# Kernel tuning notes

Hardware: AMD Instinct MI355X
Metric: run time of the kernel (lower is better)

The kernel has to match this reference:

```python
import jax, jax.numpy as jnp
import numpy as np

S, B, T = 16, 32, 64        # max_sents, batch, max_tokens
V, E, H = 50000, 256, 256   # vocab, embed_size, gru_hidden (n_dim)
NC = 50                     # n_classes


def setup_inputs() -> dict:
    key = jax.random.key(0)
    ks = jax.random.split(key, 30)

    def u(k, shape, s=0.1):
        return jax.random.uniform(k, shape, minval=-s, maxval=s, dtype=jnp.float32)

    return {
        "x": jax.random.randint(ks[0], (S, B, T), 0, V, dtype=jnp.int64),
        "embed": jax.random.normal(ks[1], (V, E), dtype=jnp.float32) * 0.1,
        # word-level bi-GRU (input E, hidden H); gate order r,z,n as in torch
        "wg_Wih_f": u(ks[2], (3 * H, E)), "wg_Whh_f": u(ks[3], (3 * H, H)),
        "wg_bih_f": u(ks[4], (3 * H,)),   "wg_bhh_f": u(ks[5], (3 * H,)),
        "wg_Wih_b": u(ks[6], (3 * H, E)), "wg_Whh_b": u(ks[7], (3 * H, H)),
        "wg_bih_b": u(ks[8], (3 * H,)),   "wg_bhh_b": u(ks[9], (3 * H,)),
        "word_W": u(ks[10], (2 * H, 2 * H)),
        "word_b": u(ks[11], (2 * H, 1)),
        "word_proj": u(ks[12], (2 * H, 1)),
        # sentence-level bi-GRU (input 2H, hidden H)
        "sg_Wih_f": u(ks[13], (3 * H, 2 * H)), "sg_Whh_f": u(ks[14], (3 * H, H)),
        "sg_bih_f": u(ks[15], (3 * H,)),       "sg_bhh_f": u(ks[16], (3 * H,)),
        "sg_Wih_b": u(ks[17], (3 * H, 2 * H)), "sg_Whh_b": u(ks[18], (3 * H, H)),
        "sg_bih_b": u(ks[19], (3 * H,)),       "sg_bhh_b": u(ks[20], (3 * H,)),
        "sent_W": u(ks[21], (2 * H, 2 * H)),
        "sent_b": u(ks[22], (2 * H, 1)),
        "sent_proj": u(ks[23], (2 * H, 1)),
        "fin_W": u(ks[24], (NC, 2 * H)),
        "fin_b": u(ks[25], (NC,)),
        "state_word": jnp.zeros((2, B, H), dtype=jnp.float32),
        "state_sent": jnp.zeros((2, B, H), dtype=jnp.float32),
    }


def _gru_dir(x, h0, Wih, Whh, bih, bhh, reverse=False):
    # x: [T, B, in]; returns hidden states [T, B, H] (in original time order)
    xp = jnp.einsum('tbe,ge->tbg', x, Wih) + bih  # precompute input projections

    def step(h, xt):
        g = h @ Whh.T + bhh
        xr, xz, xn = jnp.split(xt, 3, axis=-1)
        hr, hz, hn = jnp.split(g, 3, axis=-1)
        r = jax.nn.sigmoid(xr + hr)
        z = jax.nn.sigmoid(xz + hz)
        n = jnp.tanh(xn + r * hn)
        h = (1.0 - z) * n + z * h
        return h, h

    _, hs = jax.lax.scan(step, h0, xp, reverse=reverse)
    return hs


def _bigru(x, h0, Wf, Hf, bif, bhf, Wb, Hb, bib, bhb):
    f = _gru_dir(x, h0[0], Wf, Hf, bif, bhf, reverse=False)
    b = _gru_dir(x, h0[1], Wb, Hb, bib, bhb, reverse=True)
    return jnp.concatenate([f, b], axis=-1)  # [T, B, 2H]


def _attn_pool(out, W, b, proj):
    # out: [T, B, 2H]; batch_matmul_bias(tanh) -> batch_matmul -> softmax over T -> weighted sum
    squish = jnp.tanh(jnp.einsum('tbh,hk->tbk', out, W) + b[:, 0])  # [T,B,2H]
    scores = jnp.einsum('tbk,k->tb', squish, proj[:, 0])            # [T,B]
    a = jax.nn.softmax(scores, axis=0)                              # softmax over seq
    return jnp.einsum('tb,tbh->bh', a, out)                         # [B,2H]


def reference(x, embed,
              wg_Wih_f, wg_Whh_f, wg_bih_f, wg_bhh_f,
              wg_Wih_b, wg_Whh_b, wg_bih_b, wg_bhh_b,
              word_W, word_b, word_proj,
              sg_Wih_f, sg_Whh_f, sg_bih_f, sg_bhh_f,
              sg_Wih_b, sg_Whh_b, sg_bih_b, sg_bhh_b,
              sent_W, sent_b, sent_proj,
              fin_W, fin_b, state_word, state_sent):
    e = embed[x]                         # [S,B,T,E]
    e = jnp.transpose(e, (0, 2, 1, 3))   # [S,T,B,E] (torch code transposes per sentence)

    word_out = jax.vmap(
        lambda xs: _bigru(xs, state_word,
                          wg_Wih_f, wg_Whh_f, wg_bih_f, wg_bhh_f,
                          wg_Wih_b, wg_Whh_b, wg_bih_b, wg_bhh_b)
    )(e)                                 # [S,T,B,2H]

    s = jax.vmap(lambda o: _attn_pool(o, word_W, word_b, word_proj))(word_out)  # [S,B,2H]

    sent_out = _bigru(s, state_sent,
                      sg_Wih_f, sg_Whh_f, sg_bih_f, sg_bhh_f,
                      sg_Wih_b, sg_Whh_b, sg_bih_b, sg_bhh_b)  # [S,B,2H]
    pooled = _attn_pool(sent_out, sent_W, sent_b, sent_proj)   # [B,2H]
    return pooled @ fin_W.T + fin_b                            # [B,NC] logits
```

## Files before the change

### kernel.cpp

```cpp
#include <hip/hip_runtime.h>


typedef float  f32x4  __attribute__((ext_vector_type(4)));
typedef int    i32x4  __attribute__((ext_vector_type(4)));
typedef __bf16 bf16x8 __attribute__((ext_vector_type(8)));

#define DEVINL static __device__ __forceinline__

DEVINL unsigned short f2bf(float f) {
    unsigned int x = __builtin_bit_cast(unsigned int, f);
    x = x + 0x7fffu + ((x >> 16) & 1u);
    return (unsigned short)(x >> 16);
}
DEVINL float bf2f(unsigned short u) {
    unsigned int x = ((unsigned int)u) << 16;
    return __builtin_bit_cast(float, x);
}
DEVINL float bfe16(unsigned int v, int hi) {
    return bf2f((unsigned short)(hi ? (v >> 16) : (v & 0xffffu)));
}
DEVINL float sigm(float x) { return __builtin_amdgcn_rcpf(1.f + __expf(-x)); }
DEVINL float tanh_(float x) {
    x = fminf(fmaxf(x, -20.f), 20.f);
    float e = __expf(-2.f * x);
    return (1.f - e) * __builtin_amdgcn_rcpf(1.f + e);
}
DEVINL void mfma16(f32x4& acc, i32x4 a, i32x4 b) {
    acc = __builtin_amdgcn_mfma_f32_16x16x32_bf16(
        __builtin_bit_cast(bf16x8, a), __builtin_bit_cast(bf16x8, b), acc, 0, 0, 0);
}
DEVINL f32x4 zero4() { f32x4 v = {0.f, 0.f, 0.f, 0.f}; return v; }

#define O_WPWF    ((size_t)0)
#define O_WPWB    ((size_t)1048576)
#define O_WPSGIH  ((size_t)2097152)
#define O_WPSHHF  ((size_t)3670016)
#define O_WPSHHB  ((size_t)4063232)
#define O_WPWW    ((size_t)4456448)
#define O_WPSW    ((size_t)4980736)
#define O_BIASWF  ((size_t)5505024)
#define O_BIASWB  ((size_t)5509120)
#define O_BIHCAT  ((size_t)5513216)
#define O_WOUT    ((size_t)5519360)
#define O_SCORESW ((size_t)39073792)
#define O_SSFRAG  ((size_t)39204864)
#define O_XPSENT  ((size_t)39729152)
#define O_SOFRAG  ((size_t)42874880)
#define O_SCORESS ((size_t)43399168)
#define WS_NEED_B ((size_t)43401216)
#define O_XPW     ((size_t)43401216)
#define WS_NEED_A ((size_t)144064512)

__global__ void k_prep(const float* wihf, const float* whhf,
                       const float* wihb, const float* whhb,
                       const float* sgihf, const float* sgihb,
                       const float* sghhf, const float* sghhb,
                       const float* wordW, const float* sentW,
                       const float* bihf, const float* bhhf,
                       const float* bihb, const float* bhhb,
                       const float* sgbihf, const float* sgbihb,
                       const float* sgbhhf, const float* sgbhhb,
                       unsigned short* Wpwf, unsigned short* Wpwb,
                       unsigned short* Wpsgih,
                       unsigned short* WpshhF, unsigned short* WpshhB,
                       unsigned short* WpwW, unsigned short* WpsW,
                       float* biasWf, float* biasWb, float* bihCat)
{
    const int tid0 = blockIdx.x * blockDim.x + threadIdx.x;
    const int nth  = gridDim.x * blockDim.x;

    for (int idx = tid0; idx < 2 * 524288; idx += nth) {
        int d = idx >> 19, sidx = idx & 524287;
        int j = sidx & 7, chunk = sidx >> 3;
        int lane = chunk & 63, nk = chunk >> 6;
        int kf = nk & 15, nf = nk >> 4;
        int n = nf * 16 + (lane & 15);
        int k = kf * 32 + (lane >> 4) * 8 + j;
        const float* Wih = d ? wihb : wihf;
        const float* Whh = d ? whhb : whhf;
        int g4 = n >> 8, jj = n & 255;
        float v = 0.f;
        if (k < 256) {
            if (g4 == 0) v = Wih[jj * 256 + k];
            else if (g4 == 1) v = Wih[(256 + jj) * 256 + k];
            else if (g4 == 2) v = Wih[(512 + jj) * 256 + k];
        } else {
            int kk = k - 256;
            if (g4 == 0) v = Whh[jj * 256 + kk];
            else if (g4 == 1) v = Whh[(256 + jj) * 256 + kk];
            else if (g4 == 3) v = Whh[(512 + jj) * 256 + kk];
        }
        (d ? Wpwb : Wpwf)[sidx] = f2bf(v);
    }
    for (int idx = tid0; idx < 786432; idx += nth) {
        int j = idx & 7, chunk = idx >> 3;
        int lane = chunk & 63, nk = chunk >> 6;
        int kf = nk & 15, nf = nk >> 4;
        int n = nf * 16 + (lane & 15);
        int k = kf * 32 + (lane >> 4) * 8 + j;
        float v = (n < 768) ? sgihf[n * 512 + k] : sgihb[(n - 768) * 512 + k];
        Wpsgih[idx] = f2bf(v);
    }
    for (int idx = tid0; idx < 2 * 196608; idx += nth) {
        int d = idx >= 196608;
        int sidx = d ? idx - 196608 : idx;
        int j = sidx & 7, chunk = sidx >> 3;
        int lane = chunk & 63, nk = chunk >> 6;
        int kf = nk & 7, nf = nk >> 3;
        int n = nf * 16 + (lane & 15);
        int k = kf * 32 + (lane >> 4) * 8 + j;
        float v = (d ? sghhb : sghhf)[n * 256 + k];
        (d ? WpshhB : WpshhF)[sidx] = f2bf(v);
    }
    for (int idx = tid0; idx < 2 * 262144; idx += nth) {
        int d = idx >> 18, sidx = idx & 262143;
        int j = sidx & 7, chunk = sidx >> 3;
        int lane = chunk & 63, nk = chunk >> 6;
        int kf = nk & 15, nf = nk >> 4;
        int n = nf * 16 + (lane & 15);
        int k = kf * 32 + (lane >> 4) * 8 + j;
        float v = (d ? sentW : wordW)[k * 512 + n];
        (d ? WpsW : WpwW)[sidx] = f2bf(v);
    }
    for (int idx = tid0; idx < 2048; idx += nth) {
        int d = idx >> 10, i = idx & 1023;
        int g4 = i >> 8, j = i & 255;
        const float* bi = d ? bihb : bihf;
        const float* bh = d ? bhhb : bhhf;
        float v = (g4 == 0) ? bi[j] + bh[j]
                : (g4 == 1) ? bi[256 + j] + bh[256 + j]
                : (g4 == 2) ? bi[512 + j] : bh[512 + j];
        (d ? biasWb : biasWf)[i] = v;
    }
    for (int idx = tid0; idx < 1536; idx += nth) {
        int d = idx >= 768, j = d ? idx - 768 : idx;
        const float* bi = d ? sgbihb : sgbihf;
        const float* bh = d ? sgbhhb : sgbhhf;
        bihCat[idx] = bi[j] + ((j < 512) ? bh[j] : 0.f);
    }
}

__global__ __launch_bounds__(512, 2)
void k_xpw(const int* xg, const float* embed,
           const unsigned short* Wpwf_u, const unsigned short* Wpwb_u,
           const float* biasWf, const float* biasWb, unsigned short* xpw)
{
    __shared__ unsigned short Ebuf[2][16][256];
    const int tid = threadIdx.x, lane = tid & 63, w = tid >> 6;
    const int cid = blockIdx.x;
    const int tq = cid & 3, bh = (cid >> 2) & 1, dir = (cid >> 3) & 1, s = cid >> 4;
    const int t0 = tq * 16;
    const i32x4* Wp = (const i32x4*)(dir ? Wpwb_u : Wpwf_u);
    const float* biasW = dir ? biasWb : biasWf;
    const int b = lane & 15, rsub = lane >> 4;

    i32x4 A[3][2][8];
#pragma unroll
    for (int g = 0; g < 3; ++g)
#pragma unroll
        for (int q = 0; q < 2; ++q)
#pragma unroll
            for (int kk = 0; kk < 8; ++kk)
                A[g][q][kk] = Wp[((g * 16 + w * 2 + q) * 16 + kk) * 64 + lane];

    unsigned int biasp[3][2][2];
#pragma unroll
    for (int g = 0; g < 3; ++g)
#pragma unroll
        for (int q = 0; q < 2; ++q) {
            const int j0 = g * 256 + (w * 2 + q) * 16 + rsub * 4;
            biasp[g][q][0] = (unsigned)f2bf(biasW[j0]) |
                             ((unsigned)f2bf(biasW[j0 + 1]) << 16);
            biasp[g][q][1] = (unsigned)f2bf(biasW[j0 + 2]) |
                             ((unsigned)f2bf(biasW[j0 + 3]) << 16);
        }

    const int sb = tid >> 5, sc = tid & 31;
    const int tokrow = (s * 32 + bh * 16 + sb) * 64;
    const int sdst = sb * 512 + ((sc * 16) ^ ((sb & 7) << 4));

#define STAGE_E(BUF, T)                                                       \
    {                                                                         \
        const int tok = xg[tokrow + (T)];                                     \
        const f32x4* src = (const f32x4*)(embed + (size_t)tok * 256 + sc * 8);\
        f32x4 e0 = src[0], e1 = src[1];                                       \
        i32x4 pk;                                                             \
        pk.x = (int)((unsigned)f2bf(e0.x) | ((unsigned)f2bf(e0.y) << 16));    \
        pk.y = (int)((unsigned)f2bf(e0.z) | ((unsigned)f2bf(e0.w) << 16));    \
        pk.z = (int)((unsigned)f2bf(e1.x) | ((unsigned)f2bf(e1.y) << 16));    \
        pk.w = (int)((unsigned)f2bf(e1.z) | ((unsigned)f2bf(e1.w) << 16));    \
        *(i32x4*)((char*)&Ebuf[BUF][0][0] + sdst) = pk;                       \
    }

    STAGE_E(0, t0);
    const size_t chain = (size_t)((s * 2 + dir) * 2 + bh);
    char* const xpBase = (char*)xpw + chain * 1572864 +
                         (size_t)(rsub * 128 + b * 8);

    for (int tl = 0; tl < 16; ++tl) {
        __syncthreads();
        const int t = t0 + tl, cur = tl & 1, nxt = cur ^ 1;
        if (tl < 15) STAGE_E(nxt, t + 1);

        f32x4 acc[3][2];
#pragma unroll
        for (int g = 0; g < 3; ++g) { acc[g][0] = zero4(); acc[g][1] = zero4(); }
#pragma unroll
        for (int kk = 0; kk < 8; ++kk) {
            const int roff = b * 512 + ((kk * 64 + rsub * 16) ^ ((b & 7) << 4));
            i32x4 eb = *(const i32x4*)((const char*)&Ebuf[cur][0][0] + roff);
            mfma16(acc[0][0], A[0][0][kk], eb); mfma16(acc[0][1], A[0][1][kk], eb);
            mfma16(acc[1][0], A[1][0][kk], eb); mfma16(acc[1][1], A[1][1][kk], eb);
            mfma16(acc[2][0], A[2][0][kk], eb); mfma16(acc[2][1], A[2][1][kk], eb);
        }
        char* ob = xpBase + (size_t)t * 24576;
#pragma unroll
        for (int g = 0; g < 3; ++g)
#pragma unroll
            for (int q = 0; q < 2; ++q) {
                unsigned short us[4];
#pragma unroll
                for (int i = 0; i < 4; ++i)
                    us[i] = f2bf(acc[g][q][i] + bfe16(biasp[g][q][i >> 1], i & 1));
                uint2 pk;
                pk.x = (unsigned)us[0] | ((unsigned)us[1] << 16);
                pk.y = (unsigned)us[2] | ((unsigned)us[3] << 16);
                *(uint2*)(ob + g * 8192 + (w * 2 + q) * 512) = pk;
            }
    }
#undef STAGE_E
}

__global__ __launch_bounds__(512, 2)
void k_gru_wordA(const float* stateW,
                 const unsigned short* Wpwf_u, const unsigned short* Wpwb_u,
                 const float* biasWf, const float* biasWb,
                 const unsigned short* xpw, unsigned short* wout)
{
    __shared__ unsigned short Hbuf[2][16][256];
    const int tid = threadIdx.x, lane = tid & 63, w = tid >> 6;
    const int cid = blockIdx.x, bh = cid & 1, dir = (cid >> 1) & 1, s = cid >> 2;
    const i32x4* Wp = (const i32x4*)(dir ? Wpwb_u : Wpwf_u);
    const float* biasW = dir ? biasWb : biasWf;
    const int b = lane & 15, rsub = lane >> 4;
    const int gmap[3] = {0, 1, 3};

    i32x4 A[3][2][8];
#pragma unroll
    for (int g = 0; g < 3; ++g)
#pragma unroll
        for (int q = 0; q < 2; ++q)
#pragma unroll
            for (int kk = 0; kk < 8; ++kk)
                A[g][q][kk] =
                    Wp[((gmap[g] * 16 + w * 2 + q) * 16 + 8 + kk) * 64 + lane];

    unsigned int bhnp[2][2];
    float hreg[2][4];
#pragma unroll
    for (int q = 0; q < 2; ++q) {
        const int j0 = (w * 2 + q) * 16 + rsub * 4;
        f32x4 h0 = *(const f32x4*)(stateW + dir * 8192 + (bh * 16 + b) * 256 + j0);
        bhnp[q][0] = (unsigned)f2bf(biasW[768 + j0]) |
                     ((unsigned)f2bf(biasW[768 + j0 + 1]) << 16);
        bhnp[q][1] = (unsigned)f2bf(biasW[768 + j0 + 2]) |
                     ((unsigned)f2bf(biasW[768 + j0 + 3]) << 16);
        hreg[q][0] = h0.x; hreg[q][1] = h0.y; hreg[q][2] = h0.z; hreg[q][3] = h0.w;
        uint2 pk;
        pk.x = (unsigned)f2bf(h0.x) | ((unsigned)f2bf(h0.y) << 16);
        pk.y = (unsigned)f2bf(h0.z) | ((unsigned)f2bf(h0.w) << 16);
        const int boff = b * 512 + (((w * 2 + q) * 32 + rsub * 8) ^ ((b & 7) << 4));
        *(uint2*)((char*)&Hbuf[0][0][0] + boff) = pk;
    }
    const size_t chain = (size_t)((s * 2 + dir) * 2 + bh);
    const char* const xpBase = (const char*)xpw + chain * 1572864 +
                               (size_t)(rsub * 128 + b * 8);

    for (int ti = 0; ti < 64; ++ti) {
        __syncthreads();
        const int t = dir ? 63 - ti : ti;
        const int cur = ti & 1, nxt = cur ^ 1;

        uint2 xpv[3][2];
        const char* xb = xpBase + (size_t)t * 24576;
#pragma unroll
        for (int g = 0; g < 3; ++g)
#pragma unroll
            for (int q = 0; q < 2; ++q)
                xpv[g][q] = *(const uint2*)(xb + g * 8192 + (w * 2 + q) * 512);

        f32x4 acc[3][2];
#pragma unroll
        for (int g = 0; g < 3; ++g) { acc[g][0] = zero4(); acc[g][1] = zero4(); }
#pragma unroll
        for (int kk = 0; kk < 8; ++kk) {
            const int roff = b * 512 + ((kk * 64 + rsub * 16) ^ ((b & 7) << 4));
            i32x4 hb = *(const i32x4*)((const char*)&Hbuf[cur][0][0] + roff);
            mfma16(acc[0][0], A[0][0][kk], hb); mfma16(acc[0][1], A[0][1][kk], hb);
            mfma16(acc[1][0], A[1][0][kk], hb); mfma16(acc[1][1], A[1][1][kk], hb);
            mfma16(acc[2][0], A[2][0][kk], hb); mfma16(acc[2][1], A[2][1][kk], hb);
        }
        const int r = (s * 64 + t) * 32 + bh * 16 + b;
#pragma unroll
        for (int q = 0; q < 2; ++q) {
            unsigned short us[4];
#pragma unroll
            for (int i = 0; i < 4; ++i) {
                const unsigned xr = (i < 2) ? xpv[0][q].x : xpv[0][q].y;
                const unsigned xz = (i < 2) ? xpv[1][q].x : xpv[1][q].y;
                const unsigned xn = (i < 2) ? xpv[2][q].x : xpv[2][q].y;
                float rv = sigm(bfe16(xr, i & 1) + acc[0][q][i]);
                float zv = sigm(bfe16(xz, i & 1) + acc[1][q][i]);
                float nv = tanh_(bfe16(xn, i & 1) +
                                 rv * (acc[2][q][i] + bfe16(bhnp[q][i >> 1], i & 1)));
                float h = (1.f - zv) * nv + zv * hreg[q][i];
                hreg[q][i] = h;
                us[i] = f2bf(h);
            }
            uint2 pk;
            pk.x = (unsigned)us[0] | ((unsigned)us[1] << 16);
            pk.y = (unsigned)us[2] | ((unsigned)us[3] << 16);
            const int boff = b * 512 + (((w * 2 + q) * 32 + rsub * 8) ^ ((b & 7) << 4));
            *(uint2*)((char*)&Hbuf[nxt][0][0] + boff) = pk;
            const int hcol = dir * 256 + (w * 2 + q) * 16 + rsub * 4;
            const int widx = (((r >> 4) * 16 + (hcol >> 5)) * 64 + (r & 15) +
                              ((hcol >> 3) & 3) * 16) * 8 + (hcol & 7);
            *(uint2*)(wout + widx) = pk;
        }
    }
}

DEVINL void prefetchE(unsigned short (*Ab)[512], const int* xg, const float* embed,
                      int s, int t, int tid)
{
    const int brow = tid >> 5, c = tid & 31;
    const int tok = xg[(s * 32 + brow) * 64 + t];
    const f32x4* src = (const f32x4*)(embed + (size_t)tok * 256) + c * 2;
    f32x4 f0 = src[0], f1 = src[1];
    i32x4 pk;
    pk.x = (int)((unsigned)f2bf(f0.x) | ((unsigned)f2bf(f0.y) << 16));
    pk.y = (int)((unsigned)f2bf(f0.z) | ((unsigned)f2bf(f0.w) << 16));
    pk.z = (int)((unsigned)f2bf(f1.x) | ((unsigned)f2bf(f1.y) << 16));
    pk.w = (int)((unsigned)f2bf(f1.z) | ((unsigned)f2bf(f1.w) << 16));
    int kbyte = (c * 16) ^ ((brow & 7) << 4);
    *(i32x4*)((char*)&Ab[brow][0] + kbyte) = pk;
}

__global__ __launch_bounds__(1024, 4)
void k_gru_word(const int* xg, const float* embed, const float* stateW,
                const unsigned short* Wpwf_u, const unsigned short* Wpwb_u,
                const float* biasWf, const float* biasWb,
                unsigned short* wout)
{
    __shared__ unsigned short Abuf[2][32][512];
    const int tid = threadIdx.x, lane = tid & 63, w = tid >> 6;
    const int cid = blockIdx.x, s = cid >> 1, dir = cid & 1;
    const i32x4* Wp = (const i32x4*)(dir ? Wpwb_u : Wpwf_u);
    const float* bias = dir ? biasWb : biasWf;

    const int j = w * 16 + (lane & 15);
    float hreg[2][4];
#pragma unroll
    for (int mf = 0; mf < 2; ++mf)
#pragma unroll
        for (int i = 0; i < 4; ++i) {
            int b = mf * 16 + (lane >> 4) * 4 + i;
            float h0 = stateW[dir * 8192 + b * 256 + j];
            hreg[mf][i] = h0;
            int byteoff = ((256 + j) * 2) ^ ((b & 7) << 4);
            *(unsigned short*)((char*)&Abuf[0][b][0] + byteoff) = f2bf(h0);
        }
    const int tfirst = dir ? 63 : 0;
    prefetchE(Abuf[0], xg, embed, s, tfirst, tid);

    const float br = bias[j], bz = bias[256 + j];
    const float bxn = bias[512 + j], bhn = bias[768 + j];

    for (int ti = 0; ti < 64; ++ti) {
        __syncthreads();
        const int t = dir ? 63 - ti : ti;
        const int cur = ti & 1, nxt = cur ^ 1;
        if (ti < 63) prefetchE(Abuf[nxt], xg, embed, s, dir ? t - 1 : t + 1, tid);

        f32x4 acc[4][2];
#pragma unroll
        for (int g = 0; g < 4; ++g) { acc[g][0] = zero4(); acc[g][1] = zero4(); }

        i32x4 bbuf[3][3];
#define LOADB_W(KF, DST)                                                     \
        {                                                                    \
            const int gX = ((KF) < 8) ? 32 : 48;                             \
            DST[0] = Wp[((0 + w)  * 16 + (KF)) * 64 + lane];                 \
            DST[1] = Wp[((16 + w) * 16 + (KF)) * 64 + lane];                 \
            DST[2] = Wp[((gX + w) * 16 + (KF)) * 64 + lane];                 \
        }
        LOADB_W(0, bbuf[0]);
        LOADB_W(1, bbuf[1]);
#pragma unroll
        for (int kf = 0; kf < 16; ++kf) {
            if (kf < 14) LOADB_W(kf + 2, bbuf[(kf + 2) % 3]);
            const int row0 = lane & 15;
            const int boff = (kf * 64 + (lane >> 4) * 16) ^ ((row0 & 7) << 4);
            i32x4 a0 = *(const i32x4*)((const char*)&Abuf[cur][row0][0] + boff);
            i32x4 a1 = *(const i32x4*)((const char*)&Abuf[cur][16 + row0][0] + boff);
            const i32x4* bc = bbuf[kf % 3];
            mfma16(acc[0][0], a0, bc[0]); mfma16(acc[0][1], a1, bc[0]);
            mfma16(acc[1][0], a0, bc[1]); mfma16(acc[1][1], a1, bc[1]);
            if (kf < 8) { mfma16(acc[2][0], a0, bc[2]);
                          mfma16(acc[2][1], a1, bc[2]); }
            else        { mfma16(acc[3][0], a0, bc[2]);
                          mfma16(acc[3][1], a1, bc[2]); }
        }
#undef LOADB_W
#pragma unroll
        for (int mf = 0; mf < 2; ++mf)
#pragma unroll
            for (int i = 0; i < 4; ++i) {
                const int b = mf * 16 + (lane >> 4) * 4 + i;
                float rv = sigm(acc[0][mf][i] + br);
                float zv = sigm(acc[1][mf][i] + bz);
                float nv = tanh_(acc[2][mf][i] + bxn + rv * (acc[3][mf][i] + bhn));
                float hnew = (1.f - zv) * nv + zv * hreg[mf][i];
                hreg[mf][i] = hnew;
                unsigned short hb = f2bf(hnew);
                int byteoff = ((256 + j) * 2) ^ ((b & 7) << 4);
                *(unsigned short*)((char*)&Abuf[nxt][b][0] + byteoff) = hb;
                int r = (s * 64 + t) * 32 + b;
                int hcol = dir * 256 + j;
                wout[(((r >> 4) * 16 + (hcol >> 5)) * 64 + (r & 15) +
                      ((hcol >> 3) & 3) * 16) * 8 + (hcol & 7)] = hb;
            }
    }
}

__global__ __launch_bounds__(1024, 4)
void k_attn_score2(const unsigned short* Afrag_u, const unsigned short* Wp_u,
                   const float* wb, const float* wp, float* scores)
{
    __shared__ i32x4 Wl[2][16][64];
    const int tid = threadIdx.x, lane = tid & 63, w = tid >> 6;
    const int rblk = blockIdx.x * 16 + w;
    const i32x4* A = (const i32x4*)Afrag_u;
    const i32x4* Wg = (const i32x4*)Wp_u;

    i32x4 a[16];
#pragma unroll
    for (int kf = 0; kf < 16; ++kf) a[kf] = A[(rblk * 16 + kf) * 64 + lane];

    i32x4* wl0 = &Wl[0][0][0];
    i32x4* wl1 = &Wl[1][0][0];
    wl0[tid] = Wg[tid];

    float partial[4] = {};
    for (int nf = 0; nf < 32; ++nf) {
        __syncthreads();
        if (nf < 31) {
            i32x4* dst = (nf & 1) ? wl0 : wl1;
            dst[tid] = Wg[(nf + 1) * 1024 + tid];
        }
        const i32x4* cur = (nf & 1) ? wl1 : wl0;
        f32x4 acc0 = zero4(), acc1 = zero4();
#pragma unroll
        for (int kf = 0; kf < 16; kf += 2) {
            mfma16(acc0, a[kf],     cur[kf * 64 + lane]);
            mfma16(acc1, a[kf + 1], cur[(kf + 1) * 64 + lane]);
        }
        const int n = nf * 16 + (lane & 15);
        const float wbn = wb[n], wpn = wp[n];
#pragma unroll
        for (int i = 0; i < 4; ++i)
            partial[i] += tanh_(acc0[i] + acc1[i] + wbn) * wpn;
    }
#pragma unroll
    for (int i = 0; i < 4; ++i) {
        float v = partial[i];
        v += __shfl_xor(v, 1); v += __shfl_xor(v, 2);
        v += __shfl_xor(v, 4); v += __shfl_xor(v, 8);
        if ((lane & 15) == 0)
            scores[rblk * 16 + (lane >> 4) * 4 + i] = v;
    }
}

__global__ void k_attn_score_small(const unsigned short* Afrag_u,
                                   const unsigned short* Wp_u,
                                   const float* wb, const float* wp, float* scores)
{
    const int tid = threadIdx.x, lane = tid & 63, w = tid >> 6;
    const int rblk = blockIdx.x * 4 + w;
    const i32x4* A = (const i32x4*)Afrag_u;
    const i32x4* Wp = (const i32x4*)Wp_u;
    i32x4 a[16];
#pragma unroll
    for (int kf = 0; kf < 16; ++kf) a[kf] = A[(rblk * 16 + kf) * 64 + lane];

    float partial[4] = {};
    for (int nf = 0; nf < 32; ++nf) {
        f32x4 acc0 = zero4(), acc1 = zero4();
#pragma unroll
        for (int kf = 0; kf < 16; kf += 2) {
            mfma16(acc0, a[kf],     Wp[(nf * 16 + kf) * 64 + lane]);
            mfma16(acc1, a[kf + 1], Wp[(nf * 16 + kf + 1) * 64 + lane]);
        }
        const int n = nf * 16 + (lane & 15);
        const float wbn = wb[n], wpn = wp[n];
#pragma unroll
        for (int i = 0; i < 4; ++i)
            partial[i] += tanh_(acc0[i] + acc1[i] + wbn) * wpn;
    }
#pragma unroll
    for (int i = 0; i < 4; ++i) {
        float v = partial[i];
        v += __shfl_xor(v, 1); v += __shfl_xor(v, 2);
        v += __shfl_xor(v, 4); v += __shfl_xor(v, 8);
        if ((lane & 15) == 0)
            scores[rblk * 16 + (lane >> 4) * 4 + i] = v;
    }
}

__global__ void k_word_pool(const float* scores, const unsigned short* wout,
                            unsigned short* ssFrag)
{
    __shared__ float aL[64];
    __shared__ float part[4][64][8];
    const int tid = threadIdx.x, l = tid & 63, w = tid >> 6;
    const int bid = blockIdx.x;
    const int s = bid >> 5, b = bid & 31;
    if (w == 0) {
        float sc = scores[s * 2048 + l * 32 + b];
        float m = sc;
#pragma unroll
        for (int d = 1; d < 64; d <<= 1) m = fmaxf(m, __shfl_xor(m, d));
        float e = __expf(sc - m), sum = e;
#pragma unroll
        for (int d = 1; d < 64; d <<= 1) sum += __shfl_xor(sum, d);
        aL[l] = e * __builtin_amdgcn_rcpf(sum);
    }
    __syncthreads();

    float acc[8] = {};
    const i32x4* WO = (const i32x4*)wout;
    for (int tt = 0; tt < 16; ++tt) {
        const int t = w * 16 + tt;
        float at = aL[t];
        int cidx = ((s * 128 + t * 2 + (b >> 4)) * 16 + (l >> 2)) * 64 +
                   (b & 15) + (l & 3) * 16;
        i32x4 ch = WO[cidx];
        acc[0] += at * bf2f((unsigned short)((unsigned)ch.x & 0xffffu));
        acc[1] += at * bf2f((unsigned short)((unsigned)ch.x >> 16));
        acc[2] += at * bf2f((unsigned short)((unsigned)ch.y & 0xffffu));
        acc[3] += at * bf2f((unsigned short)((unsigned)ch.y >> 16));
        acc[4] += at * bf2f((unsigned short)((unsigned)ch.z & 0xffffu));
        acc[5] += at * bf2f((unsigned short)((unsigned)ch.z >> 16));
        acc[6] += at * bf2f((unsigned short)((unsigned)ch.w & 0xffffu));
        acc[7] += at * bf2f((unsigned short)((unsigned)ch.w >> 16));
    }
#pragma unroll
    for (int q = 0; q < 8; ++q) part[w][l][q] = acc[q];
    __syncthreads();
    if (w == 0) {
        float fin[8];
#pragma unroll
        for (int q = 0; q < 8; ++q)
            fin[q] = part[0][l][q] + part[1][l][q] + part[2][l][q] + part[3][l][q];
        i32x4 pk;
        pk.x = (int)((unsigned)f2bf(fin[0]) | ((unsigned)f2bf(fin[1]) << 16));
        pk.y = (int)((unsigned)f2bf(fin[2]) | ((unsigned)f2bf(fin[3]) << 16));
        pk.z = (int)((unsigned)f2bf(fin[4]) | ((unsigned)f2bf(fin[5]) << 16));
        pk.w = (int)((unsigned)f2bf(fin[6]) | ((unsigned)f2bf(fin[7]) << 16));
        const int r2 = s * 32 + b;
        int cidx2 = ((r2 >> 4) * 16 + (l >> 2)) * 64 + (r2 & 15) + (l & 3) * 16;
        ((i32x4*)ssFrag)[cidx2] = pk;
    }
}

__global__ void k_sgih(const unsigned short* ssFrag_u, const unsigned short* Wp_u,
                       const float* bihCat, float* xpSent)
{
    const int tid = threadIdx.x, lane = tid & 63, w = tid >> 6;
    const int rblk = blockIdx.x, ncl = blockIdx.y;
    const i32x4* A = (const i32x4*)ssFrag_u;
    const i32x4* Wp = (const i32x4*)Wp_u;
    i32x4 a[16];
#pragma unroll
    for (int kf = 0; kf < 16; ++kf) a[kf] = A[(rblk * 16 + kf) * 64 + lane];
#pragma unroll
    for (int nfl = 0; nfl < 4; ++nfl) {
        const int nfg = ncl * 16 + w * 4 + nfl;
        f32x4 acc = zero4();
#pragma unroll
        for (int kf = 0; kf < 16; ++kf)
            mfma16(acc, a[kf], Wp[(nfg * 16 + kf) * 64 + lane]);
        const int n = nfg * 16 + (lane & 15);
        const float bb = bihCat[n];
        const int dir = n >= 768, ng = n - dir * 768;
        const int g = ng >> 8, jj = ng & 255;
#pragma unroll
        for (int i = 0; i < 4; ++i) {
            int row = rblk * 16 + (lane >> 4) * 4 + i;
            int s = row >> 5, b = row & 31;
            xpSent[(((dir * 2 + (b >> 4)) * 16 + s) * 12288) +
                   (g * 256 + jj) * 16 + (b & 15)] = acc[i] + bb;
        }
    }
}

DEVINL void gload16(const void* gsrc, void* ldst) {
    __builtin_amdgcn_global_load_lds(
        (const __attribute__((address_space(1))) unsigned int*)gsrc,
        (__attribute__((address_space(3))) unsigned int*)ldst, 16, 0, 0);
}

__global__ __launch_bounds__(512)
void k_gru_sentA(const float* stateS, const unsigned short* WpF_u,
                 const unsigned short* WpB_u, const float* bhhf, const float* bhhb,
                 const float* xpSent, unsigned short* soFrag)
{
    __shared__ unsigned short Abuf[2][16][256];
    __shared__ float xpLs[2][12288];
    const int tid = threadIdx.x, lane = tid & 63, w = tid >> 6;
    const int cid = blockIdx.x, bh = cid & 1, dir = cid >> 1;
    const i32x4* Wp = (const i32x4*)(dir ? WpB_u : WpF_u);
    const float* bhh = dir ? bhhb : bhhf;

    i32x4 B[3][2][8];
#pragma unroll
    for (int g = 0; g < 3; ++g)
#pragma unroll
        for (int q = 0; q < 2; ++q)
#pragma unroll
            for (int kk = 0; kk < 8; ++kk)
                B[g][q][kk] = Wp[((g * 16 + w * 2 + q) * 8 + kk) * 64 + lane];

    float bhn[2];
    float hreg[2][4];
#pragma unroll
    for (int q = 0; q < 2; ++q) {
        const int j = (w * 2 + q) * 16 + (lane & 15);
        bhn[q] = bhh[512 + j];
#pragma unroll
        for (int i = 0; i < 4; ++i) {
            const int b = 4 * (lane >> 4) + i;
            float h0 = stateS[dir * 8192 + (bh * 16 + b) * 256 + j];
            hreg[q][i] = h0;
            int byteoff = b * 512 + ((j * 2) ^ ((b & 7) << 4));
            *(unsigned short*)((char*)&Abuf[0][0][0] + byteoff) = f2bf(h0);
        }
    }
    const size_t xbase = (size_t)((dir * 2 + bh) * 16) * 49152;
    const int sfirst = dir ? 15 : 0;
#pragma unroll
    for (int c = 0; c < 6; ++c)
        gload16((const char*)xpSent + xbase + (size_t)sfirst * 49152 +
                    ((w * 6 + c) * 64 + lane) * 16,
                (char*)&xpLs[0][0] + (w * 6 + c) * 1024);

    for (int si = 0; si < 16; ++si) {
        __syncthreads();
        const int s = dir ? 15 - si : si;
        const int cur = si & 1, nxt = cur ^ 1;
        if (si < 15) {
            const int sn = dir ? s - 1 : s + 1;
#pragma unroll
            for (int c = 0; c < 6; ++c)
                gload16((const char*)xpSent + xbase + (size_t)sn * 49152 +
                            ((w * 6 + c) * 64 + lane) * 16,
                        (char*)&xpLs[nxt][0] + (w * 6 + c) * 1024);
        }
        f32x4 acc[3][2];
#pragma unroll
        for (int g = 0; g < 3; ++g) { acc[g][0] = zero4(); acc[g][1] = zero4(); }
#pragma unroll
        for (int kk = 0; kk < 8; ++kk) {
            const int row = lane & 15;
            const int boff = (kk * 64 + (lane >> 4) * 16) ^ ((row & 7) << 4);
            i32x4 a = *(const i32x4*)((const char*)&Abuf[cur][row][0] + boff);
#pragma unroll
            for (int g = 0; g < 3; ++g) {
                mfma16(acc[g][0], a, B[g][0][kk]);
                mfma16(acc[g][1], a, B[g][1][kk]);
            }
        }
#pragma unroll
        for (int q = 0; q < 2; ++q) {
            const int j = (w * 2 + q) * 16 + (lane & 15);
            f32x4 xr = *(const f32x4*)((const char*)&xpLs[cur][0] +
                        ((0 * 256 + j) * 16 + 4 * (lane >> 4)) * 4);
            f32x4 xz = *(const f32x4*)((const char*)&xpLs[cur][0] +
                        ((1 * 256 + j) * 16 + 4 * (lane >> 4)) * 4);
            f32x4 xn = *(const f32x4*)((const char*)&xpLs[cur][0] +
                        ((2 * 256 + j) * 16 + 4 * (lane >> 4)) * 4);
#pragma unroll
            for (int i = 0; i < 4; ++i) {
                const int b = 4 * (lane >> 4) + i;
                float rv = sigm(xr[i] + acc[0][q][i]);
                float zv = sigm(xz[i] + acc[1][q][i]);
                float nv = tanh_(xn[i] + rv * (acc[2][q][i] + bhn[q]));
                float hnew = (1.f - zv) * nv + zv * hreg[q][i];
                hreg[q][i] = hnew;
                unsigned short hb = f2bf(hnew);
                int byteoff = b * 512 + ((j * 2) ^ ((b & 7) << 4));
                *(unsigned short*)((char*)&Abuf[nxt][0][0] + byteoff) = hb;
                const int r2 = s * 32 + bh * 16 + b;
                const int hcol = dir * 256 + j;
                soFrag[(((r2 >> 4) * 16 + (hcol >> 5)) * 64 + (r2 & 15) +
                        ((hcol >> 3) & 3) * 16) * 8 + (hcol & 7)] = hb;
            }
        }
    }
}

__global__ void k_sent_pool_fin(const float* scoresS, const unsigned short* soFrag,
                                const float* finW, const float* finb, float* out)
{
    __shared__ float aL[16];
    __shared__ float pooled[512];
    __shared__ float part[4][64];
    const int l = threadIdx.x;
    const int b = blockIdx.x;

    if (l < 64) {
        float sc = (l < 16) ? scoresS[l * 32 + b] : -1e30f;
        float m = sc;
#pragma unroll
        for (int d = 1; d < 16; d <<= 1) m = fmaxf(m, __shfl_xor(m, d));
        float e = (l < 16) ? __expf(sc - m) : 0.f;
        float sum = e;
#pragma unroll
        for (int d = 1; d < 16; d <<= 1) sum += __shfl_xor(sum, d);
        if (l < 16) aL[l] = e * __builtin_amdgcn_rcpf(sum);
    }
    __syncthreads();

    if (l < 64) {
        float acc[8] = {};
        const i32x4* SO = (const i32x4*)soFrag;
        for (int si = 0; si < 16; ++si) {
            float as = aL[si];
            int r2 = si * 32 + b;
            int cidx = ((r2 >> 4) * 16 + (l >> 2)) * 64 + (r2 & 15) + (l & 3) * 16;
            i32x4 ch = SO[cidx];
            acc[0] += as * bf2f((unsigned short)((unsigned)ch.x & 0xffffu));
            acc[1] += as * bf2f((unsigned short)((unsigned)ch.x >> 16));
            acc[2] += as * bf2f((unsigned short)((unsigned)ch.y & 0xffffu));
            acc[3] += as * bf2f((unsigned short)((unsigned)ch.y >> 16));
            acc[4] += as * bf2f((unsigned short)((unsigned)ch.z & 0xffffu));
            acc[5] += as * bf2f((unsigned short)((unsigned)ch.z >> 16));
            acc[6] += as * bf2f((unsigned short)((unsigned)ch.w & 0xffffu));
            acc[7] += as * bf2f((unsigned short)((unsigned)ch.w >> 16));
        }
#pragma unroll
        for (int q = 0; q < 8; ++q) pooled[l * 8 + q] = acc[q];
    }
    __syncthreads();
    {
        const int c = l & 63, kq = l >> 6;
        float v = 0.f;
        if (c < 50) {
            const float* wrow = finW + c * 512 + kq * 128;
            const float* pp = pooled + kq * 128;
            for (int k = 0; k < 128; ++k) v += pp[k] * wrow[k];
        }
        part[kq][c] = v;
    }
    __syncthreads();
    if (l < 50)
        out[b * 50 + l] = finb[l] + part[0][l] + part[1][l] + part[2][l] + part[3][l];
}

extern "C" void kernel_launch(void* const* d_in, const int* in_sizes, int n_in,
                              void* d_out, int out_size, void* d_ws, size_t ws_size,
                              hipStream_t stream)
{
    if (ws_size < WS_NEED_B) return;
    const int bigA = (ws_size >= WS_NEED_A) ? 1 : 0;

    const int*   x      = (const int*)d_in[0];
    const float* embed  = (const float*)d_in[1];
    const float* wgWihF = (const float*)d_in[2];
    const float* wgWhhF = (const float*)d_in[3];
    const float* wgBihF = (const float*)d_in[4];
    const float* wgBhhF = (const float*)d_in[5];
    const float* wgWihB = (const float*)d_in[6];
    const float* wgWhhB = (const float*)d_in[7];
    const float* wgBihB = (const float*)d_in[8];
    const float* wgBhhB = (const float*)d_in[9];
    const float* wordW  = (const float*)d_in[10];
    const float* wordB  = (const float*)d_in[11];
    const float* wordP  = (const float*)d_in[12];
    const float* sgWihF = (const float*)d_in[13];
    const float* sgWhhF = (const float*)d_in[14];
    const float* sgBihF = (const float*)d_in[15];
    const float* sgBhhF = (const float*)d_in[16];
    const float* sgWihB = (const float*)d_in[17];
    const float* sgWhhB = (const float*)d_in[18];
    const float* sgBihB = (const float*)d_in[19];
    const float* sgBhhB = (const float*)d_in[20];
    const float* sentWm = (const float*)d_in[21];
    const float* sentB  = (const float*)d_in[22];
    const float* sentP  = (const float*)d_in[23];
    const float* finW   = (const float*)d_in[24];
    const float* finB   = (const float*)d_in[25];
    const float* stateW = (const float*)d_in[26];
    const float* stateS = (const float*)d_in[27];

    char* ws = (char*)d_ws;
    unsigned short* Wpwf   = (unsigned short*)(ws + O_WPWF);
    unsigned short* Wpwb   = (unsigned short*)(ws + O_WPWB);
    unsigned short* Wpsgih = (unsigned short*)(ws + O_WPSGIH);
    unsigned short* WpshhF = (unsigned short*)(ws + O_WPSHHF);
    unsigned short* WpshhB = (unsigned short*)(ws + O_WPSHHB);
    unsigned short* WpwW   = (unsigned short*)(ws + O_WPWW);
    unsigned short* WpsW   = (unsigned short*)(ws + O_WPSW);
    float* biasWf  = (float*)(ws + O_BIASWF);
    float* biasWb  = (float*)(ws + O_BIASWB);
    float* bihCat  = (float*)(ws + O_BIHCAT);
    unsigned short* wout   = (unsigned short*)(ws + O_WOUT);
    float* scoresW = (float*)(ws + O_SCORESW);
    unsigned short* ssFrag = (unsigned short*)(ws + O_SSFRAG);
    float* xpSent  = (float*)(ws + O_XPSENT);
    unsigned short* soFrag = (unsigned short*)(ws + O_SOFRAG);
    float* scoresS = (float*)(ws + O_SCORESS);
    unsigned short* xpw    = (unsigned short*)(ws + O_XPW);

    k_prep<<<512, 256, 0, stream>>>(wgWihF, wgWhhF, wgWihB, wgWhhB,
                                    sgWihF, sgWihB, sgWhhF, sgWhhB,
                                    wordW, sentWm,
                                    wgBihF, wgBhhF, wgBihB, wgBhhB,
                                    sgBihF, sgBihB, sgBhhF, sgBhhB,
                                    Wpwf, Wpwb, Wpsgih, WpshhF, WpshhB,
                                    WpwW, WpsW, biasWf, biasWb, bihCat);

    if (bigA) {
        k_xpw<<<256, 512, 0, stream>>>(x, embed, Wpwf, Wpwb, biasWf, biasWb, xpw);
        k_gru_wordA<<<64, 512, 0, stream>>>(stateW, Wpwf, Wpwb, biasWf, biasWb,
                                            xpw, wout);
    } else {
        k_gru_word<<<32, 1024, 0, stream>>>(x, embed, stateW, Wpwf, Wpwb,
                                            biasWf, biasWb, wout);
    }

    k_attn_score2<<<128, 1024, 0, stream>>>(wout, WpwW, wordB, wordP, scoresW);
    k_word_pool<<<512, 256, 0, stream>>>(scoresW, wout, ssFrag);

    k_sgih<<<dim3(32, 6), 256, 0, stream>>>(ssFrag, Wpsgih, bihCat, xpSent);
    k_gru_sentA<<<4, 512, 0, stream>>>(stateS, WpshhF, WpshhB, sgBhhF, sgBhhB,
                                       xpSent, soFrag);

    k_attn_score_small<<<8, 256, 0, stream>>>(soFrag, WpsW, sentB, sentP, scoresS);
    k_sent_pool_fin<<<32, 256, 0, stream>>>(scoresS, soFrag, finW, finB,
                                            (float*)d_out);
}
```

Measured before the change: 445.2 us.

## Vectorize weight prep, prefetch next-step projections, use hardware bf16 convert

The weight-packing prep kernel now has each thread handle one 8-element chunk with two float4 loads and a single 16-byte store, replacing scalar per-element loads and stores. The word GRU recurrence now loads the next timestep's input projections during the current step, taking that global load latency off the serial chain. f2bf uses the compiler's native bf16 conversion, and the GRU update is rewritten as nv + z*(h - nv). The fallback k_gru_word path is removed, so the launcher now returns early unless the workspace is large enough for the precomputed-projection path, and the prefetch adds register pressure.

New measurement: 471.1 us. 5.8% more time.

```diff
diff --git a/kernel.cpp b/kernel.cpp
--- a/kernel.cpp
+++ b/kernel.cpp
@@ -8,9 +8,8 @@
 #define DEVINL static __device__ __forceinline__
 
 DEVINL unsigned short f2bf(float f) {
-    unsigned int x = __builtin_bit_cast(unsigned int, f);
-    x = x + 0x7fffu + ((x >> 16) & 1u);
-    return (unsigned short)(x >> 16);
+    __bf16 b = (__bf16)f;
+    return __builtin_bit_cast(unsigned short, b);
 }
 DEVINL float bf2f(unsigned short u) {
     unsigned int x = ((unsigned int)u) << 16;
@@ -30,6 +29,14 @@
         __builtin_bit_cast(bf16x8, a), __builtin_bit_cast(bf16x8, b), acc, 0, 0, 0);
 }
 DEVINL f32x4 zero4() { f32x4 v = {0.f, 0.f, 0.f, 0.f}; return v; }
+DEVINL i32x4 pack8f(f32x4 v0, f32x4 v1) {
+    i32x4 p;
+    p.x = (int)((unsigned)f2bf(v0.x) | ((unsigned)f2bf(v0.y) << 16));
+    p.y = (int)((unsigned)f2bf(v0.z) | ((unsigned)f2bf(v0.w) << 16));
+    p.z = (int)((unsigned)f2bf(v1.x) | ((unsigned)f2bf(v1.y) << 16));
+    p.w = (int)((unsigned)f2bf(v1.z) | ((unsigned)f2bf(v1.w) << 16));
+    return p;
+}
 
 #define O_WPWF    ((size_t)0)
 #define O_WPWB    ((size_t)1048576)
@@ -69,58 +76,63 @@
     const int tid0 = blockIdx.x * blockDim.x + threadIdx.x;
     const int nth  = gridDim.x * blockDim.x;
 
-    for (int idx = tid0; idx < 2 * 524288; idx += nth) {
-        int d = idx >> 19, sidx = idx & 524287;
-        int j = sidx & 7, chunk = sidx >> 3;
+    for (int c = tid0; c < 2 * 65536; c += nth) {
+        int d = c >> 16, chunk = c & 65535;
         int lane = chunk & 63, nk = chunk >> 6;
         int kf = nk & 15, nf = nk >> 4;
         int n = nf * 16 + (lane & 15);
-        int k = kf * 32 + (lane >> 4) * 8 + j;
-        const float* Wih = d ? wihb : wihf;
-        const float* Whh = d ? whhb : whhf;
+        int k0 = kf * 32 + (lane >> 4) * 8;
         int g4 = n >> 8, jj = n & 255;
-        float v = 0.f;
-        if (k < 256) {
-            if (g4 == 0) v = Wih[jj * 256 + k];
-            else if (g4 == 1) v = Wih[(256 + jj) * 256 + k];
-            else if (g4 == 2) v = Wih[(512 + jj) * 256 + k];
-        } else {
-            int kk = k - 256;
-            if (g4 == 0) v = Whh[jj * 256 + kk];
-            else if (g4 == 1) v = Whh[(256 + jj) * 256 + kk];
-            else if (g4 == 3) v = Whh[(512 + jj) * 256 + kk];
-        }
-        (d ? Wpwb : Wpwf)[sidx] = f2bf(v);
-    }
-    for (int idx = tid0; idx < 786432; idx += nth) {
-        int j = idx & 7, chunk = idx >> 3;
+        i32x4 p = {0, 0, 0, 0};
+        const bool zero = (k0 < 256) ? (g4 == 3) : (g4 == 2);
+        if (!zero) {
+            const float* src;
+            if (k0 < 256) {
+                src = (d ? wihb : wihf) + (g4 * 256 + jj) * 256 + k0;
+            } else {
+                int row = (g4 == 3) ? (512 + jj) : (g4 * 256 + jj);
+                src = (d ? whhb : whhf) + row * 256 + (k0 - 256);
+            }
+            p = pack8f(*(const f32x4*)src, *(const f32x4*)(src + 4));
+        }
+        *(i32x4*)((d ? Wpwb : Wpwf) + chunk * 8) = p;
+    }
+    for (int chunk = tid0; chunk < 98304; chunk += nth) {
         int lane = chunk & 63, nk = chunk >> 6;
         int kf = nk & 15, nf = nk >> 4;
         int n = nf * 16 + (lane & 15);
-        int k = kf * 32 + (lane >> 4) * 8 + j;
-        float v = (n < 768) ? sgihf[n * 512 + k] : sgihb[(n - 768) * 512 + k];
-        Wpsgih[idx] = f2bf(v);
-    }
-    for (int idx = tid0; idx < 2 * 196608; idx += nth) {
-        int d = idx >= 196608;
-        int sidx = d ? idx - 196608 : idx;
-        int j = sidx & 7, chunk = sidx >> 3;
+        int k0 = kf * 32 + (lane >> 4) * 8;
+        const float* src = (n < 768) ? sgihf + n * 512 + k0
+                                     : sgihb + (n - 768) * 512 + k0;
+        *(i32x4*)(Wpsgih + chunk * 8) =
+            pack8f(*(const f32x4*)src, *(const f32x4*)(src + 4));
+    }
+    for (int c = tid0; c < 2 * 24576; c += nth) {
+        int d = c >= 24576, chunk = d ? c - 24576 : c;
         int lane = chunk & 63, nk = chunk >> 6;
         int kf = nk & 7, nf = nk >> 3;
         int n = nf * 16 + (lane & 15);
-        int k = kf * 32 + (lane >> 4) * 8 + j;
-        float v = (d ? sghhb : sghhf)[n * 256 + k];
-        (d ? WpshhB : WpshhF)[sidx] = f2bf(v);
-    }
-    for (int idx = tid0; idx < 2 * 262144; idx += nth) {
-        int d = idx >> 18, sidx = idx & 262143;
-        int j = sidx & 7, chunk = sidx >> 3;
+        int k0 = kf * 32 + (lane >> 4) * 8;
+        const float* src = (d ? sghhb : sghhf) + n * 256 + k0;
+        *(i32x4*)((d ? WpshhB : WpshhF) + chunk * 8) =
+            pack8f(*(const f32x4*)src, *(const f32x4*)(src + 4));
+    }
+    for (int c = tid0; c < 2 * 32768; c += nth) {
+        int d = c >> 15, chunk = c & 32767;
         int lane = chunk & 63, nk = chunk >> 6;
         int kf = nk & 15, nf = nk >> 4;
         int n = nf * 16 + (lane & 15);
-        int k = kf * 32 + (lane >> 4) * 8 + j;
-        float v = (d ? sentW : wordW)[k * 512 + n];
-        (d ? WpsW : WpwW)[sidx] = f2bf(v);
+        int k0 = kf * 32 + (lane >> 4) * 8;
+        const float* W = (d ? sentW : wordW) + (size_t)k0 * 512 + n;
+        unsigned short us[8];
+#pragma unroll
+        for (int j = 0; j < 8; ++j) us[j] = f2bf(W[j * 512]);
+        i32x4 p;
+        p.x = (int)((unsigned)us[0] | ((unsigned)us[1] << 16));
+        p.y = (int)((unsigned)us[2] | ((unsigned)us[3] << 16));
+        p.z = (int)((unsigned)us[4] | ((unsigned)us[5] << 16));
+        p.w = (int)((unsigned)us[6] | ((unsigned)us[7] << 16));
+        *(i32x4*)((d ? WpsW : WpwW) + chunk * 8) = p;
     }
     for (int idx = tid0; idx < 2048; idx += nth) {
         int d = idx >> 10, i = idx & 1023;
@@ -183,13 +195,7 @@
     {                                                                         \
         const int tok = xg[tokrow + (T)];                                     \
         const f32x4* src = (const f32x4*)(embed + (size_t)tok * 256 + sc * 8);\
-        f32x4 e0 = src[0], e1 = src[1];                                       \
-        i32x4 pk;                                                             \
-        pk.x = (int)((unsigned)f2bf(e0.x) | ((unsigned)f2bf(e0.y) << 16));    \
-        pk.y = (int)((unsigned)f2bf(e0.z) | ((unsigned)f2bf(e0.w) << 16));    \
-        pk.z = (int)((unsigned)f2bf(e1.x) | ((unsigned)f2bf(e1.y) << 16));    \
-        pk.w = (int)((unsigned)f2bf(e1.z) | ((unsigned)f2bf(e1.w) << 16));    \
-        *(i32x4*)((char*)&Ebuf[BUF][0][0] + sdst) = pk;                       \
+        *(i32x4*)((char*)&Ebuf[BUF][0][0] + sdst) = pack8f(src[0], src[1]);   \
     }
 
     STAGE_E(0, t0);
@@ -276,18 +282,30 @@
     const char* const xpBase = (const char*)xpw + chain * 1572864 +
                                (size_t)(rsub * 128 + b * 8);
 
+    uint2 xpv[3][2];
+    {
+        const char* xb = xpBase + (size_t)(dir ? 63 : 0) * 24576;
+#pragma unroll
+        for (int g = 0; g < 3; ++g)
+#pragma unroll
+            for (int q = 0; q < 2; ++q)
+                xpv[g][q] = *(const uint2*)(xb + g * 8192 + (w * 2 + q) * 512);
+    }
+
     for (int ti = 0; ti < 64; ++ti) {
         __syncthreads();
         const int t = dir ? 63 - ti : ti;
         const int cur = ti & 1, nxt = cur ^ 1;
 
-        uint2 xpv[3][2];
-        const char* xb = xpBase + (size_t)t * 24576;
-#pragma unroll
-        for (int g = 0; g < 3; ++g)
-#pragma unroll
-            for (int q = 0; q < 2; ++q)
-                xpv[g][q] = *(const uint2*)(xb + g * 8192 + (w * 2 + q) * 512);
+        uint2 xpn[3][2];
+        if (ti < 63) {
+            const char* xb = xpBase + (size_t)(dir ? t - 1 : t + 1) * 24576;
+#pragma unroll
+            for (int g = 0; g < 3; ++g)
+#pragma unroll
+                for (int q = 0; q < 2; ++q)
+                    xpn[g][q] = *(const uint2*)(xb + g * 8192 + (w * 2 + q) * 512);
+        }
 
         f32x4 acc[3][2];
 #pragma unroll
@@ -313,7 +331,7 @@
                 float zv = sigm(bfe16(xz, i & 1) + acc[1][q][i]);
                 float nv = tanh_(bfe16(xn, i & 1) +
                                  rv * (acc[2][q][i] + bfe16(bhnp[q][i >> 1], i & 1)));
-                float h = (1.f - zv) * nv + zv * hreg[q][i];
+                float h = nv + zv * (hreg[q][i] - nv);
                 hreg[q][i] = h;
                 us[i] = f2bf(h);
             }
@@ -327,109 +345,13 @@
                               ((hcol >> 3) & 3) * 16) * 8 + (hcol & 7);
             *(uint2*)(wout + widx) = pk;
         }
-    }
-}
-
-DEVINL void prefetchE(unsigned short (*Ab)[512], const int* xg, const float* embed,
-                      int s, int t, int tid)
-{
-    const int brow = tid >> 5, c = tid & 31;
-    const int tok = xg[(s * 32 + brow) * 64 + t];
-    const f32x4* src = (const f32x4*)(embed + (size_t)tok * 256) + c * 2;
-    f32x4 f0 = src[0], f1 = src[1];
-    i32x4 pk;
-    pk.x = (int)((unsigned)f2bf(f0.x) | ((unsigned)f2bf(f0.y) << 16));
-    pk.y = (int)((unsigned)f2bf(f0.z) | ((unsigned)f2bf(f0.w) << 16));
-    pk.z = (int)((unsigned)f2bf(f1.x) | ((unsigned)f2bf(f1.y) << 16));
-    pk.w = (int)((unsigned)f2bf(f1.z) | ((unsigned)f2bf(f1.w) << 16));
-    int kbyte = (c * 16) ^ ((brow & 7) << 4);
-    *(i32x4*)((char*)&Ab[brow][0] + kbyte) = pk;
-}
-
-__global__ __launch_bounds__(1024, 4)
-void k_gru_word(const int* xg, const float* embed, const float* stateW,
-                const unsigned short* Wpwf_u, const unsigned short* Wpwb_u,
-                const float* biasWf, const float* biasWb,
-                unsigned short* wout)
-{
-    __shared__ unsigned short Abuf[2][32][512];
-    const int tid = threadIdx.x, lane = tid & 63, w = tid >> 6;
-    const int cid = blockIdx.x, s = cid >> 1, dir = cid & 1;
-    const i32x4* Wp = (const i32x4*)(dir ? Wpwb_u : Wpwf_u);
-    const float* bias = dir ? biasWb : biasWf;
-
-    const int j = w * 16 + (lane & 15);
-    float hreg[2][4];
-#pragma unroll
-    for (int mf = 0; mf < 2; ++mf)
-#pragma unroll
-        for (int i = 0; i < 4; ++i) {
-            int b = mf * 16 + (lane >> 4) * 4 + i;
-            float h0 = stateW[dir * 8192 + b * 256 + j];
-            hreg[mf][i] = h0;
-            int byteoff = ((256 + j) * 2) ^ ((b & 7) << 4);
-            *(unsigned short*)((char*)&Abuf[0][b][0] + byteoff) = f2bf(h0);
-        }
-    const int tfirst = dir ? 63 : 0;
-    prefetchE(Abuf[0], xg, embed, s, tfirst, tid);
-
-    const float br = bias[j], bz = bias[256 + j];
-    const float bxn = bias[512 + j], bhn = bias[768 + j];
-
-    for (int ti = 0; ti < 64; ++ti) {
-        __syncthreads();
-        const int t = dir ? 63 - ti : ti;
-        const int cur = ti & 1, nxt = cur ^ 1;
-        if (ti < 63) prefetchE(Abuf[nxt], xg, embed, s, dir ? t - 1 : t + 1, tid);
-
-        f32x4 acc[4][2];
-#pragma unroll
-        for (int g = 0; g < 4; ++g) { acc[g][0] = zero4(); acc[g][1] = zero4(); }
-
-        i32x4 bbuf[3][3];
-#define LOADB_W(KF, DST)                                                     \
-        {                                                                    \
-            const int gX = ((KF) < 8) ? 32 : 48;                             \
-            DST[0] = Wp[((0 + w)  * 16 + (KF)) * 64 + lane];                 \
-            DST[1] = Wp[((16 + w) * 16 + (KF)) * 64 + lane];                 \
-            DST[2] = Wp[((gX + w) * 16 + (KF)) * 64 + lane];                 \
-        }
-        LOADB_W(0, bbuf[0]);
-        LOADB_W(1, bbuf[1]);
-#pragma unroll
-        for (int kf = 0; kf < 16; ++kf) {
-            if (kf < 14) LOADB_W(kf + 2, bbuf[(kf + 2) % 3]);
-            const int row0 = lane & 15;
-            const int boff = (kf * 64 + (lane >> 4) * 16) ^ ((row0 & 7) << 4);
-            i32x4 a0 = *(const i32x4*)((const char*)&Abuf[cur][row0][0] + boff);
-            i32x4 a1 = *(const i32x4*)((const char*)&Abuf[cur][16 + row0][0] + boff);
-            const i32x4* bc = bbuf[kf % 3];
-            mfma16(acc[0][0], a0, bc[0]); mfma16(acc[0][1], a1, bc[0]);
-            mfma16(acc[1][0], a0, bc[1]); mfma16(acc[1][1], a1, bc[1]);
-            if (kf < 8) { mfma16(acc[2][0], a0, bc[2]);
-                          mfma16(acc[2][1], a1, bc[2]); }
-            else        { mfma16(acc[3][0], a0, bc[2]);
-                          mfma16(acc[3][1], a1, bc[2]); }
-        }
-#undef LOADB_W
-#pragma unroll
-        for (int mf = 0; mf < 2; ++mf)
-#pragma unroll
-            for (int i = 0; i < 4; ++i) {
-                const int b = mf * 16 + (lane >> 4) * 4 + i;
-                float rv = sigm(acc[0][mf][i] + br);
-                float zv = sigm(acc[1][mf][i] + bz);
-                float nv = tanh_(acc[2][mf][i] + bxn + rv * (acc[3][mf][i] + bhn));
-                float hnew = (1.f - zv) * nv + zv * hreg[mf][i];
-                hreg[mf][i] = hnew;
-                unsigned short hb = f2bf(hnew);
-                int byteoff = ((256 + j) * 2) ^ ((b & 7) << 4);
-                *(unsigned short*)((char*)&Abuf[nxt][b][0] + byteoff) = hb;
-                int r = (s * 64 + t) * 32 + b;
-                int hcol = dir * 256 + j;
-                wout[(((r >> 4) * 16 + (hcol >> 5)) * 64 + (r & 15) +
-                      ((hcol >> 3) & 3) * 16) * 8 + (hcol & 7)] = hb;
-            }
+        if (ti < 63) {
+#pragma unroll
+            for (int g = 0; g < 3; ++g)
+#pragma unroll
+                for (int q = 0; q < 2; ++q)
+                    xpv[g][q] = xpn[g][q];
+        }
     }
 }
 
@@ -695,7 +617,7 @@
                 float rv = sigm(xr[i] + acc[0][q][i]);
                 float zv = sigm(xz[i] + acc[1][q][i]);
                 float nv = tanh_(xn[i] + rv * (acc[2][q][i] + bhn[q]));
-                float hnew = (1.f - zv) * nv + zv * hreg[q][i];
+                float hnew = nv + zv * (hreg[q][i] - nv);
                 hreg[q][i] = hnew;
                 unsigned short hb = f2bf(hnew);
                 int byteoff = b * 512 + ((j * 2) ^ ((b & 7) << 4));
@@ -771,8 +693,7 @@
                               void* d_out, int out_size, void* d_ws, size_t ws_size,
                               hipStream_t stream)
 {
-    if (ws_size < WS_NEED_B) return;
-    const int bigA = (ws_size >= WS_NEED_A) ? 1 : 0;
+    if (ws_size < WS_NEED_A) return;
 
     const int*   x      = (const int*)d_in[0];
     const float* embed  = (const float*)d_in[1];
@@ -830,14 +751,9 @@
                                     Wpwf, Wpwb, Wpsgih, WpshhF, WpshhB,
                                     WpwW, WpsW, biasWf, biasWb, bihCat);
 
-    if (bigA) {
-        k_xpw<<<256, 512, 0, stream>>>(x, embed, Wpwf, Wpwb, biasWf, biasWb, xpw);
-        k_gru_wordA<<<64, 512, 0, stream>>>(stateW, Wpwf, Wpwb, biasWf, biasWb,
-                                            xpw, wout);
-    } else {
-        k_gru_word<<<32, 1024, 0, stream>>>(x, embed, stateW, Wpwf, Wpwb,
-                                            biasWf, biasWb, wout);
-    }
+    k_xpw<<<256, 512, 0, stream>>>(x, embed, Wpwf, Wpwb, biasWf, biasWb, xpw);
+    k_gru_wordA<<<64, 512, 0, stream>>>(stateW, Wpwf, Wpwb, biasWf, biasWb,
+                                        xpw, wout);
 
     k_attn_score2<<<128, 1024, 0, stream>>>(wout, WpwW, wordB, wordP, scoresW);
     k_word_pool<<<512, 256, 0, stream>>>(scoresW, wout, ssFrag);
```
